# Optimization experiments

Hardware: AMD Instinct MI355X
Metric: run time of the kernel (lower is better)

## Reference

```python
import jax, jax.numpy as jnp
import numpy as np

P = 16          # patch size (patch_height == patch_width)
DIM = 768       # feature dim
K = 9           # number of anchor boxes (arange(0, 9) in source)
# anchor_boxes = [(h_ratio, w_ratio) for h in (2,4,8) for w in (2,4,8)]
BOX_H = jnp.array([2., 2., 2., 4., 4., 4., 8., 8., 8.], dtype=jnp.float32)
BOX_W = jnp.array([2., 4., 8., 2., 4., 8., 2., 4., 8.], dtype=jnp.float32)


def setup_inputs() -> dict:
    key = jax.random.key(0)
    k0, k1, k2, k3 = jax.random.split(key, 4)
    b, c, h, w = 32, 3, 512, 512
    img = jax.random.normal(k0, (b, c, h, w), dtype=jnp.float32)
    # patch-embed stand-in for feature_extraction_ViT: (c*P*P) -> DIM
    w_patch = jax.random.normal(k1, (c * P * P, DIM), dtype=jnp.float32) * 0.02
    w_reg = jax.random.normal(k2, (DIM, 4 * K), dtype=jnp.float32) * 0.02
    b_reg = jnp.zeros((4 * K,), dtype=jnp.float32)
    w_obj = jax.random.normal(k3, (DIM, K), dtype=jnp.float32) * 0.02
    b_obj = jnp.zeros((K,), dtype=jnp.float32)
    return {"img": img, "w_patch": w_patch, "w_reg": w_reg, "b_reg": b_reg,
            "w_obj": w_obj, "b_obj": b_obj}


def reference(img, w_patch, w_reg, b_reg, w_obj, b_obj):
    b, c, h, w = img.shape
    fh, fw = h // P, w // P
    # --- feature_extraction_ViT (patch embedding) -> feature map [b, fh, fw, DIM]
    patches = img.reshape(b, c, fh, P, fw, P).transpose(0, 2, 4, 1, 3, 5)
    patches = patches.reshape(b, fh, fw, c * P * P)
    feat = patches @ w_patch                                  # [b, fh, fw, DIM]
    # --- RPN: regs [b, fh, fw, K, 4], objectness [b, fh, fw, K, 1]
    regs = (feat @ w_reg + b_reg).reshape(b, fh, fw, K, 4)    # separate_anchor_boxes, s=4
    is_object = jax.nn.sigmoid(feat @ w_obj + b_obj)[..., None]
    # --- anchor-box coordinate decoding (memory-bound broadcast pipeline)
    wgrid = jnp.arange(0, w, P, dtype=jnp.float32)            # step = patch_width
    hgrid = jnp.arange(0, h, P, dtype=jnp.float32)            # step = patch_height
    width_coords = wgrid[None, None, :, None, None] + regs[..., 0:1]
    height_coords = hgrid[None, :, None, None, None] + regs[..., 1:2]
    width_abs = width_coords + BOX_W[None, None, None, :, None] * regs[..., 2:3]
    height_abs = height_coords + BOX_H[None, None, None, :, None] * regs[..., 3:4]
    batch_idx = jnp.broadcast_to(
        jnp.arange(b, dtype=jnp.float32)[:, None, None, None, None], (b, fh, fw, K, 1))
    k_idx = jnp.broadcast_to(
        jnp.arange(K, dtype=jnp.float32)[None, None, None, :, None], (b, fh, fw, K, 1))
    merged = jnp.concatenate(
        [width_coords, height_coords, width_abs, height_abs, batch_idx, is_object, k_idx],
        axis=-1)                                              # [b, fh, fw, K, 7]
    tensor_reshaped = merged.reshape(-1, 7)                   # (b h w k) x
    return tensor_reshaped
```

## Files before the change

### kernel.cpp

```cpp
#include <hip/hip_runtime.h>
#include <hip/hip_bf16.h>

typedef __attribute__((ext_vector_type(8))) short bf16x8;
typedef __attribute__((ext_vector_type(4))) float f32x4;

__device__ __forceinline__ unsigned short f2bf(float f) {
    unsigned int u = __float_as_uint(f);
    u = (u + 0x7FFFu + ((u >> 16) & 1u)) >> 16;
    return (unsigned short)u;
}

__device__ __forceinline__ unsigned int pkbf(float x, float y) {
    __hip_bfloat162 h = __float22bfloat162_rn(float2{x, y});
    unsigned int u;
    __builtin_memcpy(&u, &h, 4);
    return u;
}

__global__ __launch_bounds__(512) void wcomb_fused(
        const float* __restrict__ wp, const float* __restrict__ wreg,
        const float* __restrict__ wobj, unsigned short* __restrict__ wct) {
    __shared__ float Al[8 * 384];
    __shared__ float Bw[384 * 52];

    const int t    = threadIdx.x;
    const int w    = t >> 6;
    const int lane = t & 63;
    const int kg   = blockIdx.x * 8 + w;

    float acc = 0.f;

    #pragma unroll
    for (int ch = 0; ch < 2; ++ch) {
        const int d0 = ch * 384;
        if (ch) __syncthreads();

        for (int e = t; e < 768; e += 512) {
            int r = e / 96, j = e - r * 96;
            *(f32x4*)&Al[r * 384 + j * 4] =
                *(const f32x4*)&wp[(size_t)(blockIdx.x * 8 + r) * 768 + d0 + j * 4];
        }
        for (int e = t; e < 3456; e += 512) {
            int r = e / 9, j = e - r * 9;
            *(f32x4*)&Bw[r * 52 + j * 4] =
                *(const f32x4*)&wreg[(size_t)(d0 + r) * 36 + j * 4];
        }
        for (int e = t; e < 3456; e += 512) {
            int r = e / 9, c = e - r * 9;
            Bw[r * 52 + 36 + c] = wobj[(size_t)(d0 + r) * 9 + c];
        }
        __syncthreads();

        if (lane < 45) {
            const float* alr = &Al[w * 384];
            #pragma unroll 8
            for (int j = 0; j < 96; ++j) {
                f32x4 a = *(const f32x4*)&alr[j * 4];
                acc += a.x * Bw[(j * 4 + 0) * 52 + lane]
                     + a.y * Bw[(j * 4 + 1) * 52 + lane]
                     + a.z * Bw[(j * 4 + 2) * 52 + lane]
                     + a.w * Bw[(j * 4 + 3) * 52 + lane];
            }
        }
    }

    if (lane < 45)      wct[(size_t)lane * 768 + kg] = f2bf(acc);
    else if (lane < 48) wct[(size_t)lane * 768 + kg] = 0;
}

__global__ __launch_bounds__(256) void detector_main(
        const float* __restrict__ img, const unsigned short* __restrict__ wct,
        const float* __restrict__ breg, const float* __restrict__ bobj,
        float* __restrict__ out) {
    __shared__ float Co[4][16][49];

    const int t    = threadIdx.x;
    const int lane = t & 63;
    const int wid  = t >> 6;
    const int cl   = lane & 15;
    const int q    = lane >> 4;
    const int tg   = blockIdx.x;
    const int fj0  = (tg & 1) * 16;
    const int fi   = (tg >> 1) & 31;
    const int b    = tg >> 6;
    const int k0   = wid * 6;

    const float* abase = img + (size_t)b * 786432
        + (size_t)(fi * 16 + (q >> 1)) * 512 + (fj0 + cl) * 16 + (q & 1) * 8;
    const unsigned short* bbase = wct + cl * 768 + q * 8;

    #define AOFF(kk) ((size_t)((kk) >> 3) * 262144 + (size_t)((kk) & 7) * 1024)

    f32x4 acc0 = {0.f,0.f,0.f,0.f}, acc1 = acc0, acc2 = acc0;

    f32x4 a0lo = *(const f32x4*)(abase + AOFF(k0));
    f32x4 a0hi = *(const f32x4*)(abase + AOFF(k0) + 4);
    f32x4 a1lo = *(const f32x4*)(abase + AOFF(k0 + 1));
    f32x4 a1hi = *(const f32x4*)(abase + AOFF(k0 + 1) + 4);
    bf16x8 b0x = *(const bf16x8*)(bbase + (size_t)k0 * 32);
    bf16x8 b0y = *(const bf16x8*)(bbase + (size_t)k0 * 32 + 12288);
    bf16x8 b0z = *(const bf16x8*)(bbase + (size_t)k0 * 32 + 24576);

    #pragma unroll
    for (int i = 0; i < 6; ++i) {
        f32x4 a2lo, a2hi;
        if (i < 4) {
            a2lo = *(const f32x4*)(abase + AOFF(k0 + i + 2));
            a2hi = *(const f32x4*)(abase + AOFF(k0 + i + 2) + 4);
        } else { a2lo = a1lo; a2hi = a1hi; }
        bf16x8 b1x, b1y, b1z;
        if (i < 5) {
            b1x = *(const bf16x8*)(bbase + (size_t)(k0 + i + 1) * 32);
            b1y = *(const bf16x8*)(bbase + (size_t)(k0 + i + 1) * 32 + 12288);
            b1z = *(const bf16x8*)(bbase + (size_t)(k0 + i + 1) * 32 + 24576);
        } else { b1x = b0x; b1y = b0y; b1z = b0z; }

        union { bf16x8 v; unsigned int u[4]; } af;
        af.u[0] = pkbf(a0lo.x, a0lo.y);
        af.u[1] = pkbf(a0lo.z, a0lo.w);
        af.u[2] = pkbf(a0hi.x, a0hi.y);
        af.u[3] = pkbf(a0hi.z, a0hi.w);
        acc0 = __builtin_amdgcn_mfma_f32_16x16x32_bf16(af.v, b0x, acc0, 0, 0, 0);
        acc1 = __builtin_amdgcn_mfma_f32_16x16x32_bf16(af.v, b0y, acc1, 0, 0, 0);
        acc2 = __builtin_amdgcn_mfma_f32_16x16x32_bf16(af.v, b0z, acc2, 0, 0, 0);

        a0lo = a1lo; a0hi = a1hi; a1lo = a2lo; a1hi = a2hi;
        b0x = b1x; b0y = b1y; b0z = b1z;
    }
    #undef AOFF

    #pragma unroll
    for (int r = 0; r < 4; ++r) {
        Co[wid][q * 4 + r][ 0 + cl] = acc0[r];
        Co[wid][q * 4 + r][16 + cl] = acc1[r];
        Co[wid][q * 4 + r][32 + cl] = acc2[r];
    }
    __syncthreads();

    for (int rr = t; rr < 144; rr += 256) {
        int cell = rr / 9, k = rr - cell * 9;
        int dfj  = fj0 + cell;
        float v0 = Co[0][cell][4*k+0] + Co[1][cell][4*k+0]
                 + Co[2][cell][4*k+0] + Co[3][cell][4*k+0] + breg[4*k+0];
        float v1 = Co[0][cell][4*k+1] + Co[1][cell][4*k+1]
                 + Co[2][cell][4*k+1] + Co[3][cell][4*k+1] + breg[4*k+1];
        float v2 = Co[0][cell][4*k+2] + Co[1][cell][4*k+2]
                 + Co[2][cell][4*k+2] + Co[3][cell][4*k+2] + breg[4*k+2];
        float v3 = Co[0][cell][4*k+3] + Co[1][cell][4*k+3]
                 + Co[2][cell][4*k+3] + Co[3][cell][4*k+3] + breg[4*k+3];
        float lg = Co[0][cell][36+k]  + Co[1][cell][36+k]
                 + Co[2][cell][36+k]  + Co[3][cell][36+k]  + bobj[k];
        float obj = 1.f / (1.f + __expf(-lg));
        float wc = (float)(dfj * 16) + v0;
        float hc = (float)(fi * 16) + v1;
        float wa = wc + (float)(2 << (k % 3)) * v2;
        float ha = hc + (float)(2 << (k / 3)) * v3;
        float* o = out + (size_t)(((b * 32 + fi) * 32 + dfj) * 9 + k) * 7;
        o[0] = wc; o[1] = hc; o[2] = wa; o[3] = ha;
        o[4] = (float)b; o[5] = obj; o[6] = (float)k;
    }
}

extern "C" void kernel_launch(void* const* d_in, const int* in_sizes, int n_in,
                              void* d_out, int out_size, void* d_ws, size_t ws_size,
                              hipStream_t stream) {
    const float* img  = (const float*)d_in[0];
    const float* wp   = (const float*)d_in[1];
    const float* wreg = (const float*)d_in[2];
    const float* breg = (const float*)d_in[3];
    const float* wobj = (const float*)d_in[4];
    const float* bobj = (const float*)d_in[5];
    float* out = (float*)d_out;

    unsigned short* wct = (unsigned short*)d_ws;

    wcomb_fused<<<96, 512, 0, stream>>>(wp, wreg, wobj, wct);
    detector_main<<<2048, 256, 0, stream>>>(img, wct, breg, bobj, out);
}
```

Before: 188.6 us.

## Compute combined weight matrix with bf16 MFMA after separate transpose pass

Replaces the scalar FP32 shared-memory kernel that folds the patch-embed weights into the RPN head weights. A small kernel now transposes and converts the head weights to bf16, and a second kernel runs the 768x768 by 768x48 product with MFMA instructions, splitting K across four waves and reducing the partial sums through shared memory. This shortens the weight-folding prologue, at the cost of one extra launch and extra bf16 rounding of an intermediate operand.

```diff
diff --git a/kernel.cpp b/kernel.cpp
--- a/kernel.cpp
+++ b/kernel.cpp
@@ -17,55 +17,67 @@
     return u;
 }
 
-__global__ __launch_bounds__(512) void wcomb_fused(
-        const float* __restrict__ wp, const float* __restrict__ wreg,
-        const float* __restrict__ wobj, unsigned short* __restrict__ wct) {
-    __shared__ float Al[8 * 384];
-    __shared__ float Bw[384 * 52];
+__global__ __launch_bounds__(256) void btrans_bf16(
+        const float* __restrict__ wreg, const float* __restrict__ wobj,
+        unsigned short* __restrict__ Btu) {
+    const int idx = blockIdx.x * 256 + threadIdx.x;
+    const int n = idx / 768, d = idx - n * 768;
+    float v = 0.f;
+    if (n < 36)      v = wreg[(size_t)d * 36 + n];
+    else if (n < 45) v = wobj[(size_t)d * 9 + (n - 36)];
+    Btu[idx] = f2bf(v);
+}
+
+__global__ __launch_bounds__(256) void wcomb_mfma(
+        const float* __restrict__ wp, const unsigned short* __restrict__ Btu,
+        unsigned short* __restrict__ wct) {
+    __shared__ float Co[4][16][49];
 
     const int t    = threadIdx.x;
-    const int w    = t >> 6;
     const int lane = t & 63;
-    const int kg   = blockIdx.x * 8 + w;
+    const int wid  = t >> 6;
+    const int cl   = lane & 15;
+    const int q    = lane >> 4;
+    const int kb   = blockIdx.x * 16;
 
-    float acc = 0.f;
+    const float* abase = wp + (size_t)(kb + cl) * 768 + q * 8;
+    const unsigned short* bbase = Btu + (size_t)cl * 768 + q * 8;
+    const int dw = wid * 192;
+
+    f32x4 acc0 = {0.f,0.f,0.f,0.f}, acc1 = acc0, acc2 = acc0;
 
     #pragma unroll
-    for (int ch = 0; ch < 2; ++ch) {
-        const int d0 = ch * 384;
-        if (ch) __syncthreads();
+    for (int s = 0; s < 6; ++s) {
+        const int d0 = dw + s * 32;
+        f32x4 alo = *(const f32x4*)(abase + d0);
+        f32x4 ahi = *(const f32x4*)(abase + d0 + 4);
+        bf16x8 bx = *(const bf16x8*)(bbase + d0);
+        bf16x8 by = *(const bf16x8*)(bbase + d0 + 12288);
+        bf16x8 bz = *(const bf16x8*)(bbase + d0 + 24576);
 
-        for (int e = t; e < 768; e += 512) {
-            int r = e / 96, j = e - r * 96;
-            *(f32x4*)&Al[r * 384 + j * 4] =
-                *(const f32x4*)&wp[(size_t)(blockIdx.x * 8 + r) * 768 + d0 + j * 4];
-        }
-        for (int e = t; e < 3456; e += 512) {
-            int r = e / 9, j = e - r * 9;
-            *(f32x4*)&Bw[r * 52 + j * 4] =
-                *(const f32x4*)&wreg[(size_t)(d0 + r) * 36 + j * 4];
-        }
-        for (int e = t; e < 3456; e += 512) {
-            int r = e / 9, c = e - r * 9;
-            Bw[r * 52 + 36 + c] = wobj[(size_t)(d0 + r) * 9 + c];
-        }
-        __syncthreads();
-
-        if (lane < 45) {
-            const float* alr = &Al[w * 384];
-            #pragma unroll 8
-            for (int j = 0; j < 96; ++j) {
-                f32x4 a = *(const f32x4*)&alr[j * 4];
-                acc += a.x * Bw[(j * 4 + 0) * 52 + lane]
-                     + a.y * Bw[(j * 4 + 1) * 52 + lane]
-                     + a.z * Bw[(j * 4 + 2) * 52 + lane]
-                     + a.w * Bw[(j * 4 + 3) * 52 + lane];
-            }
-        }
+        union { bf16x8 v; unsigned int u[4]; } af;
+        af.u[0] = pkbf(alo.x, alo.y);
+        af.u[1] = pkbf(alo.z, alo.w);
+        af.u[2] = pkbf(ahi.x, ahi.y);
+        af.u[3] = pkbf(ahi.z, ahi.w);
+        acc0 = __builtin_amdgcn_mfma_f32_16x16x32_bf16(af.v, bx, acc0, 0, 0, 0);
+        acc1 = __builtin_amdgcn_mfma_f32_16x16x32_bf16(af.v, by, acc1, 0, 0, 0);
+        acc2 = __builtin_amdgcn_mfma_f32_16x16x32_bf16(af.v, bz, acc2, 0, 0, 0);
     }
 
-    if (lane < 45)      wct[(size_t)lane * 768 + kg] = f2bf(acc);
-    else if (lane < 48) wct[(size_t)lane * 768 + kg] = 0;
+    #pragma unroll
+    for (int r = 0; r < 4; ++r) {
+        Co[wid][q * 4 + r][ 0 + cl] = acc0[r];
+        Co[wid][q * 4 + r][16 + cl] = acc1[r];
+        Co[wid][q * 4 + r][32 + cl] = acc2[r];
+    }
+    __syncthreads();
+
+    for (int e = t; e < 768; e += 256) {
+        int m = e / 48, n = e - m * 48;
+        float s = Co[0][m][n] + Co[1][m][n] + Co[2][m][n] + Co[3][m][n];
+        wct[(size_t)n * 768 + kb + m] = f2bf(s);
+    }
 }
 
 __global__ __launch_bounds__(256) void detector_main(
@@ -173,7 +185,9 @@
     float* out = (float*)d_out;
 
     unsigned short* wct = (unsigned short*)d_ws;
+    unsigned short* Btu = (unsigned short*)((char*)d_ws + 73728);
 
-    wcomb_fused<<<96, 512, 0, stream>>>(wp, wreg, wobj, wct);
+    btrans_bf16<<<144, 256, 0, stream>>>(wreg, wobj, Btu);
+    wcomb_mfma<<<48, 256, 0, stream>>>(wp, Btu, wct);
     detector_main<<<2048, 256, 0, stream>>>(img, wct, breg, bobj, out);
 }
```

Measured after the change: 171.3 us, median of 2. 1.1x faster.
